# Performance work log

Hardware: AMD Instinct MI355X
Metric: run time of the kernel (lower is better)

## Reference

```python
import jax, jax.numpy as jnp
import numpy as np
from jax import lax

DIM = 512          # input channels
H_IN = 56          # input spatial size
B = 32             # batch
C = DIM // 4       # inner attention dim = 128
WS = H_IN // 4     # window size = 14
NH = 4             # num_heads (C > 64 branch)
HD = C // NH       # head dim = 32
N = WS * WS        # tokens = 196
BN_EPS = 1e-5


def _rel_index():
    # Swin-style relative position index, matches the torch buffer computation.
    coords = np.stack(np.meshgrid(np.arange(WS), np.arange(WS), indexing='ij'))  # [2,WS,WS]
    flat = coords.reshape(2, -1)                                                 # [2,N]
    rel = (flat[:, :, None] - flat[:, None, :]).transpose(1, 2, 0).astype(np.int64)  # [N,N,2]
    rel[..., 0] += WS - 1
    rel[..., 1] += WS - 1
    rel[..., 0] *= 2 * WS - 1
    return jnp.asarray(rel.sum(-1))  # [N,N] int


def _interp_mat(n_in, scale):
    # Bilinear upsample (align_corners=True, as in nn.UpsamplingBilinear2d) as a matrix.
    n_out = n_in * scale
    src = np.arange(n_out) * (n_in - 1) / (n_out - 1)
    lo = np.floor(src).astype(np.int64)
    hi = np.minimum(lo + 1, n_in - 1)
    w = (src - lo).astype(np.float32)
    M = np.zeros((n_out, n_in), np.float32)
    M[np.arange(n_out), lo] += 1.0 - w
    M[np.arange(n_out), hi] += w
    return jnp.asarray(M)  # [n_out, n_in]


def setup_inputs() -> dict:
    key = jax.random.key(0)
    ks = jax.random.split(key, 8)
    x = jax.random.normal(ks[0], (B, DIM, H_IN, H_IN), jnp.float32)
    # grouped 4x4/stride-4 conv: groups = C, in_per_group = DIM // C = 4 -> OIHW [C,4,4,4]
    conv_w = jax.random.normal(ks[1], (C, 4, 4, 4), jnp.float32) * 0.05
    conv_b = jnp.zeros((C,), jnp.float32)
    bn_gamma = jnp.ones((C,), jnp.float32)
    bn_beta = jnp.zeros((C,), jnp.float32)
    bn_mean = jnp.zeros((C,), jnp.float32)
    bn_var = jnp.ones((C,), jnp.float32)
    qkv_w = jax.random.normal(ks[2], (3 * C, C), jnp.float32) * (C ** -0.5)
    proj_w = jax.random.normal(ks[3], (C, C), jnp.float32) * (C ** -0.5)
    proj_b = jnp.zeros((C,), jnp.float32)
    rpb_table = jax.random.normal(ks[4], ((2 * WS - 1) ** 2, NH), jnp.float32) * 0.02
    convout_w = jax.random.normal(ks[5], (DIM, C), jnp.float32) * (C ** -0.5)
    convout_b = jnp.zeros((DIM,), jnp.float32)
    return dict(x=x, conv_w=conv_w, conv_b=conv_b, bn_gamma=bn_gamma, bn_beta=bn_beta,
                bn_mean=bn_mean, bn_var=bn_var, qkv_w=qkv_w, proj_w=proj_w, proj_b=proj_b,
                rpb_table=rpb_table, convout_w=convout_w, convout_b=convout_b)


def reference(x, conv_w, conv_b, bn_gamma, bn_beta, bn_mean, bn_var,
              qkv_w, proj_w, proj_b, rpb_table, convout_w, convout_b):
    # local_embed: grouped conv 4x4 s4 -> BN (eval) -> ReLU6
    y = lax.conv_general_dilated(x, conv_w, window_strides=(4, 4), padding='VALID',
                                 dimension_numbers=('NCHW', 'OIHW', 'NCHW'),
                                 feature_group_count=C)
    y = y + conv_b[None, :, None, None]
    scale_bn = bn_gamma * lax.rsqrt(bn_var + BN_EPS)
    y = y * scale_bn[None, :, None, None] + (bn_beta - bn_mean * scale_bn)[None, :, None, None]
    y = jnp.clip(y, 0.0, 6.0)  # ReLU6

    # flatten to tokens: [B, N, C]
    t = y.reshape(B, C, N).transpose(0, 2, 1)

    # qkv projection (no bias) -> q,k,v [B, NH, N, HD]
    qkv = (t @ qkv_w.T).reshape(B, N, 3, NH, HD).transpose(2, 0, 3, 1, 4)
    q, k, v = qkv[0], qkv[1], qkv[2]
    q = q * (HD ** -0.5)

    attn = jnp.einsum('bhnd,bhmd->bhnm', q, k)  # [B,NH,N,N]
    idx = _rel_index()                           # [N,N]
    bias = rpb_table[idx.reshape(-1)].reshape(N, N, NH).transpose(2, 0, 1)  # [NH,N,N]
    attn = jax.nn.softmax(attn + bias[None], axis=-1)

    o = jnp.einsum('bhnm,bhmd->bhnd', attn, v)  # [B,NH,N,HD]
    o = o.transpose(0, 2, 1, 3).reshape(B, N, C)
    o = o @ proj_w.T + proj_b

    # blc2bchw
    o = o.reshape(B, WS, WS, C).transpose(0, 3, 1, 2)  # [B,C,WS,WS]

    # 1x1 conv back to DIM channels
    o = jnp.einsum('oc,bchw->bohw', convout_w, o) + convout_b[None, :, None, None]

    # bilinear upsample x4, align_corners=True
    M = _interp_mat(WS, 4)  # [4*WS, WS]
    o = jnp.einsum('Oh,bchw->bcOw', M, o)
    o = jnp.einsum('Pw,bchw->bchP', M, o)
    return o  # [B, DIM, H_IN, H_IN]
```

## Files before the change

### kernel.cpp

```cpp
#include <hip/hip_runtime.h>

#define QSCALE 0.17677669529663687f

__global__ __launch_bounds__(256) void conv_embed_kernel(
    const float* __restrict__ x, const float* __restrict__ cw,
    const float* __restrict__ cb, const float* __restrict__ gam,
    const float* __restrict__ bet, const float* __restrict__ mea,
    const float* __restrict__ var, float* __restrict__ tbuf)
{
  __shared__ __align__(16) float xs[12544];
  __shared__ __align__(16) float wsm[64];
  const int c = blockIdx.x, b = blockIdx.y, tid = threadIdx.x;
  const float4* xb = (const float4*)(x + (b*512 + 4*c)*3136);
  for (int t = tid; t < 3136; t += 256) ((float4*)xs)[t] = xb[t];
  if (tid < 64) wsm[tid] = cw[c*64 + tid];
  __syncthreads();
  if (tid < 196) {
    int oy = tid / 14, ox = tid - (tid/14)*14;
    float acc = cb[c];
#pragma unroll
    for (int i = 0; i < 4; ++i)
#pragma unroll
      for (int kh = 0; kh < 4; ++kh) {
        float4 xv = *(const float4*)&xs[i*3136 + (4*oy+kh)*56 + 4*ox];
        float4 wv = *(const float4*)&wsm[i*16 + kh*4];
        acc += xv.x*wv.x + xv.y*wv.y + xv.z*wv.z + xv.w*wv.w;
      }
    float sc = gam[c] * rsqrtf(var[c] + 1e-5f);
    float v = acc*sc + (bet[c] - mea[c]*sc);
    v = fminf(fmaxf(v, 0.0f), 6.0f);
    tbuf[(b*196 + tid)*128 + c] = v;
  }
}

__global__ __launch_bounds__(256) void make_wc_kernel(
    const float* __restrict__ cow, const float* __restrict__ pw,
    const float* __restrict__ pb, const float* __restrict__ cob,
    float* __restrict__ Wc, float* __restrict__ bias_c)
{
  int idx = blockIdx.x*256 + threadIdx.x;
  int oc = idx >> 7, k = idx & 127;
  float acc = 0.f;
  for (int cc = 0; cc < 128; ++cc) acc += cow[oc*128 + cc] * pw[cc*128 + k];
  Wc[idx] = acc;
  if (blockIdx.x < 2) {
    float a2 = cob[idx];
    for (int cc = 0; cc < 128; ++cc) a2 += cow[idx*128 + cc] * pb[cc];
    bias_c[idx] = a2;
  }
}

__device__ __forceinline__ void gemm_tile_64x64(
    const float* __restrict__ Ag, const float* __restrict__ Bg,
    int row0, int col0, float* As, float* Bs, float (&acc)[4][4])
{
  const int tid = threadIdx.x;
#pragma unroll
  for (int it = 0; it < 8; ++it) {
    int rr = (it & 3)*16 + (tid & 15);
    int kq = (it >> 2)*16 + (tid >> 4);
    float4 va = *(const float4*)&Ag[(row0+rr)*128 + kq*4];
    As[(4*kq+0)*68 + rr] = va.x;
    As[(4*kq+1)*68 + rr] = va.y;
    As[(4*kq+2)*68 + rr] = va.z;
    As[(4*kq+3)*68 + rr] = va.w;
    float4 vb = *(const float4*)&Bg[(col0+rr)*128 + kq*4];
    Bs[(4*kq+0)*68 + rr] = vb.x;
    Bs[(4*kq+1)*68 + rr] = vb.y;
    Bs[(4*kq+2)*68 + rr] = vb.z;
    Bs[(4*kq+3)*68 + rr] = vb.w;
  }
  __syncthreads();
  const int tx = (tid & 15)*4, ty = (tid >> 4)*4;
#pragma unroll 8
  for (int k = 0; k < 128; ++k) {
    float4 a4 = *(const float4*)&As[k*68 + ty];
    float4 b4 = *(const float4*)&Bs[k*68 + tx];
    float av[4] = {a4.x, a4.y, a4.z, a4.w};
    float bv[4] = {b4.x, b4.y, b4.z, b4.w};
#pragma unroll
    for (int i = 0; i < 4; ++i)
#pragma unroll
      for (int j = 0; j < 4; ++j) acc[i][j] += av[i]*bv[j];
  }
}

__global__ __launch_bounds__(256) void gemm_qkv_kernel(
    const float* __restrict__ t, const float* __restrict__ qkv_w,
    float* __restrict__ qkv)
{
  __shared__ __align__(16) float As[128*68];
  __shared__ __align__(16) float Bs[128*68];
  float acc[4][4] = {};
  gemm_tile_64x64(t, qkv_w, blockIdx.y*64, blockIdx.x*64, As, Bs, acc);
  const int tid = threadIdx.x;
  const int tx = (tid & 15)*4, ty = (tid >> 4)*4;
  const int col0 = blockIdx.x*64 + tx;
  const int s3 = col0 >> 7, rr = col0 & 127;
  const int hh = rr >> 5, dd = rr & 31;
  const float qs = (s3 == 0) ? QSCALE : 1.0f;
#pragma unroll
  for (int i = 0; i < 4; ++i) {
    int row = blockIdx.y*64 + ty + i;
    int bb = row / 196, nn = row - bb*196;
    float4 v;
    v.x = acc[i][0]*qs; v.y = acc[i][1]*qs; v.z = acc[i][2]*qs; v.w = acc[i][3]*qs;
    *(float4*)&qkv[(((s3*32 + bb)*4 + hh)*196 + nn)*32 + dd] = v;
  }
}

__global__ __launch_bounds__(256) void attn_kernel(
    const float* __restrict__ qkv, const float* __restrict__ rpb,
    float* __restrict__ o)
{
  __shared__ __align__(16) float k_lds[196*32];
  __shared__ __align__(16) float v_lds[196*32];
  __shared__ float rpb_lds[729];
  __shared__ int   off_lds[196];
  const int qhalf = blockIdx.x, h = blockIdx.y, b = blockIdx.z;
  const int tid = threadIdx.x;
  const float4* kg = (const float4*)(qkv + ((32 + b)*4 + h)*6272);
  const float4* vg = (const float4*)(qkv + ((64 + b)*4 + h)*6272);
  for (int t = tid; t < 1568; t += 256) {
    ((float4*)k_lds)[t] = kg[t];
    ((float4*)v_lds)[t] = vg[t];
  }
  for (int t = tid; t < 729; t += 256) rpb_lds[t] = rpb[t*4 + h];
  if (tid < 196) { int y = tid/14; off_lds[tid] = y*27 + (tid - y*14); }

  const int r = tid >> 1, half = tid & 1;
  const bool act = (r < 98);
  const int n = qhalf*98 + (act ? r : 0);
  const float4* qg = (const float4*)(qkv + ((b*4 + h)*196 + n)*32);
  float4 qv[8];
#pragma unroll
  for (int d = 0; d < 8; ++d) qv[d] = qg[d];
  const int yn = n/14, xn = n - yn*14;
  const int basen = yn*27 + xn + 364;
  __syncthreads();

  float mx = -1e30f, sum = 0.f;
  float4 oa[8];
#pragma unroll
  for (int d = 0; d < 8; ++d) oa[d] = make_float4(0.f, 0.f, 0.f, 0.f);
  const int m0 = half*98;
#pragma unroll 2
  for (int i = 0; i < 98; ++i) {
    const int m = m0 + i;
    const float4* kr = (const float4*)&k_lds[m*32];
    float sx = 0.f, sy = 0.f, sz = 0.f, sw = 0.f;
#pragma unroll
    for (int d = 0; d < 8; ++d) {
      float4 kv = kr[d];
      sx += qv[d].x*kv.x; sy += qv[d].y*kv.y;
      sz += qv[d].z*kv.z; sw += qv[d].w*kv.w;
    }
    float s = (sx + sy) + (sz + sw) + rpb_lds[basen - off_lds[m]];
    if (s > mx + 4.f) {
      float sc = __expf(mx - s);
      sum *= sc;
#pragma unroll
      for (int d = 0; d < 8; ++d) {
        oa[d].x *= sc; oa[d].y *= sc; oa[d].z *= sc; oa[d].w *= sc;
      }
      mx = s;
    }
    float e = __expf(s - mx);
    sum += e;
    const float4* vr = (const float4*)&v_lds[m*32];
#pragma unroll
    for (int d = 0; d < 8; ++d) {
      float4 vv = vr[d];
      oa[d].x += e*vv.x; oa[d].y += e*vv.y;
      oa[d].z += e*vv.z; oa[d].w += e*vv.w;
    }
  }
  float omx  = __shfl_xor(mx, 1);
  float osum = __shfl_xor(sum, 1);
  float M = fmaxf(mx, omx);
  float sa = __expf(mx - M), sb = __expf(omx - M);
  float inv = 1.f / (sum*sa + osum*sb);
  sa *= inv; sb *= inv;
#pragma unroll
  for (int d = 0; d < 8; ++d) {
    float px = __shfl_xor(oa[d].x, 1);
    float py = __shfl_xor(oa[d].y, 1);
    float pz = __shfl_xor(oa[d].z, 1);
    float pw = __shfl_xor(oa[d].w, 1);
    oa[d].x = oa[d].x*sa + px*sb;
    oa[d].y = oa[d].y*sa + py*sb;
    oa[d].z = oa[d].z*sa + pz*sb;
    oa[d].w = oa[d].w*sa + pw*sb;
  }
  if (act && half == 0) {
    float4* op = (float4*)&o[(b*196 + n)*128 + h*32];
#pragma unroll
    for (int d = 0; d < 8; ++d) op[d] = oa[d];
  }
}

__global__ __launch_bounds__(256) void gemm_out_kernel(
    const float* __restrict__ obuf, const float* __restrict__ Wc,
    const float* __restrict__ bias_c, float* __restrict__ co)
{
  __shared__ __align__(16) float As[128*68];
  __shared__ __align__(16) float Bs[128*68];
  float acc[4][4] = {};
  gemm_tile_64x64(obuf, Wc, blockIdx.y*64, blockIdx.x*64, As, Bs, acc);
  const int tid = threadIdx.x;
  const int tx = (tid & 15)*4, ty = (tid >> 4)*4;
  const int row0 = blockIdx.y*64 + ty;
  const int bb = row0 / 196, nn0 = row0 - bb*196;
#pragma unroll
  for (int j = 0; j < 4; ++j) {
    int col = blockIdx.x*64 + tx + j;
    float bc = bias_c[col];
    float4 v;
    v.x = acc[0][j] + bc; v.y = acc[1][j] + bc;
    v.z = acc[2][j] + bc; v.w = acc[3][j] + bc;
    *(float4*)&co[(bb*512 + col)*196 + nn0] = v;
  }
}

__global__ __launch_bounds__(256) void upsample_kernel(
    const float* __restrict__ co, float* __restrict__ out)
{
  __shared__ float cs[1568];
  __shared__ int lo_s[56];
  __shared__ float w_s[56];
  const int cg = blockIdx.x, b = blockIdx.y, tid = threadIdx.x;
  const float* cbase = co + (b*512 + cg*8)*196;
  for (int t = tid; t < 1568; t += 256) cs[t] = cbase[t];
  if (tid < 56) {
    double s = (double)(tid*13) / 55.0;
    int lo = (int)s;
    lo_s[tid] = lo;
    w_s[tid] = (float)(s - lo);
  }
  __syncthreads();
  float* obase = out + (b*512 + cg*8)*3136;
  for (int t4 = tid; t4 < 6272; t4 += 256) {
    int ch = t4 / 784;
    int rem = t4 - ch*784;
    int i2 = rem / 14;
    int j4 = (rem - i2*14)*4;
    int li = lo_s[i2]; float wi = w_s[i2];
    int hi = (li+1 < 13) ? li+1 : 13;
    const float* p0 = cs + ch*196 + li*14;
    const float* p1 = cs + ch*196 + hi*14;
    float4 ov;
    float* ovp = (float*)&ov;
#pragma unroll
    for (int jj = 0; jj < 4; ++jj) {
      int j2 = j4 + jj;
      int lj = lo_s[j2]; float wj = w_s[j2];
      int hj = (lj+1 < 13) ? lj+1 : 13;
      float top = p0[lj]*(1.f-wj) + p0[hj]*wj;
      float bot = p1[lj]*(1.f-wj) + p1[hj]*wj;
      ovp[jj] = top*(1.f-wi) + bot*wi;
    }
    ((float4*)obase)[t4] = ov;
  }
}

extern "C" void kernel_launch(void* const* d_in, const int* in_sizes, int n_in,
                              void* d_out, int out_size, void* d_ws, size_t ws_size,
                              hipStream_t stream)
{
  const float* x         = (const float*)d_in[0];
  const float* conv_w    = (const float*)d_in[1];
  const float* conv_b    = (const float*)d_in[2];
  const float* bn_gamma  = (const float*)d_in[3];
  const float* bn_beta   = (const float*)d_in[4];
  const float* bn_mean   = (const float*)d_in[5];
  const float* bn_var    = (const float*)d_in[6];
  const float* qkv_w     = (const float*)d_in[7];
  const float* proj_w    = (const float*)d_in[8];
  const float* proj_b    = (const float*)d_in[9];
  const float* rpb       = (const float*)d_in[10];
  const float* convout_w = (const float*)d_in[11];
  const float* convout_b = (const float*)d_in[12];
  float* out = (float*)d_out;
  float* ws  = (float*)d_ws;

  float* tbuf   = ws;
  float* qkvb   = ws + 802816;
  float* obuf   = ws + 3211264;
  float* Wc     = ws + 4014080;
  float* bias_c = ws + 4079616;
  float* co     = ws + 4080128;

  conv_embed_kernel<<<dim3(128, 32), 256, 0, stream>>>(
      x, conv_w, conv_b, bn_gamma, bn_beta, bn_mean, bn_var, tbuf);
  make_wc_kernel<<<dim3(256), 256, 0, stream>>>(
      convout_w, proj_w, proj_b, convout_b, Wc, bias_c);
  gemm_qkv_kernel<<<dim3(6, 98), 256, 0, stream>>>(tbuf, qkv_w, qkvb);
  attn_kernel<<<dim3(2, 4, 32), 256, 0, stream>>>(qkvb, rpb, obuf);
  gemm_out_kernel<<<dim3(8, 98), 256, 0, stream>>>(obuf, Wc, bias_c, co);
  upsample_kernel<<<dim3(64, 32), 256, 0, stream>>>(co, out);
}
```

Baseline: 482.0 us.

## Use split-bf16 MFMA for the qkv and output projection GEMMs

```diff
diff --git a/kernel.cpp b/kernel.cpp
--- a/kernel.cpp
+++ b/kernel.cpp
@@ -1,6 +1,9 @@
 #include <hip/hip_runtime.h>
 
 #define QSCALE 0.17677669529663687f
+
+typedef __attribute__((ext_vector_type(8))) short bf16x8;
+typedef __attribute__((ext_vector_type(4))) float f32x4;
 
 __global__ __launch_bounds__(256) void conv_embed_kernel(
     const float* __restrict__ x, const float* __restrict__ cw,
@@ -50,38 +53,64 @@
   }
 }
 
-__device__ __forceinline__ void gemm_tile_64x64(
+__device__ __forceinline__ unsigned short f2bf(float f)
+{
+  unsigned u = __float_as_uint(f);
+  u += 0x7fffu + ((u >> 16) & 1u);
+  return (unsigned short)(u >> 16);
+}
+
+__device__ __forceinline__ void stage64x128(
+    const float* __restrict__ g, unsigned short* hi, unsigned short* lo, int tid)
+{
+#pragma unroll
+  for (int i = 0; i < 8; ++i) {
+    int idx4 = tid + i*256;
+    int row = idx4 >> 5;
+    int c4  = idx4 & 31;
+    float4 v = *(const float4*)&g[idx4*4];
+    ushort4 h, l;
+    h.x = f2bf(v.x); h.y = f2bf(v.y); h.z = f2bf(v.z); h.w = f2bf(v.w);
+    l.x = f2bf(v.x - __uint_as_float((unsigned)h.x << 16));
+    l.y = f2bf(v.y - __uint_as_float((unsigned)h.y << 16));
+    l.z = f2bf(v.z - __uint_as_float((unsigned)h.z << 16));
+    l.w = f2bf(v.w - __uint_as_float((unsigned)h.w << 16));
+    int slot = (c4 >> 1) ^ (row & 7);
+    int uidx = row*128 + slot*8 + (c4 & 1)*4;
+    *(ushort4*)&hi[uidx] = h;
+    *(ushort4*)&lo[uidx] = l;
+  }
+}
+
+__device__ __forceinline__ bf16x8 ldfrag(const unsigned short* p, int row, int kb)
+{
+  return *(const bf16x8*)&p[row*128 + (kb ^ (row & 7))*8];
+}
+
+__device__ __forceinline__ void mfma_tile_64x64(
     const float* __restrict__ Ag, const float* __restrict__ Bg,
-    int row0, int col0, float* As, float* Bs, float (&acc)[4][4])
+    unsigned short* Ahi, unsigned short* Alo,
+    unsigned short* Bhi, unsigned short* Blo, f32x4 (&acc)[4])
 {
   const int tid = threadIdx.x;
-#pragma unroll
-  for (int it = 0; it < 8; ++it) {
-    int rr = (it & 3)*16 + (tid & 15);
-    int kq = (it >> 2)*16 + (tid >> 4);
-    float4 va = *(const float4*)&Ag[(row0+rr)*128 + kq*4];
-    As[(4*kq+0)*68 + rr] = va.x;
-    As[(4*kq+1)*68 + rr] = va.y;
-    As[(4*kq+2)*68 + rr] = va.z;
-    As[(4*kq+3)*68 + rr] = va.w;
-    float4 vb = *(const float4*)&Bg[(col0+rr)*128 + kq*4];
-    Bs[(4*kq+0)*68 + rr] = vb.x;
-    Bs[(4*kq+1)*68 + rr] = vb.y;
-    Bs[(4*kq+2)*68 + rr] = vb.z;
-    Bs[(4*kq+3)*68 + rr] = vb.w;
-  }
-  __syncthreads();
-  const int tx = (tid & 15)*4, ty = (tid >> 4)*4;
-#pragma unroll 8
-  for (int k = 0; k < 128; ++k) {
-    float4 a4 = *(const float4*)&As[k*68 + ty];
-    float4 b4 = *(const float4*)&Bs[k*68 + tx];
-    float av[4] = {a4.x, a4.y, a4.z, a4.w};
-    float bv[4] = {b4.x, b4.y, b4.z, b4.w};
-#pragma unroll
-    for (int i = 0; i < 4; ++i)
-#pragma unroll
-      for (int j = 0; j < 4; ++j) acc[i][j] += av[i]*bv[j];
+  stage64x128(Ag, Ahi, Alo, tid);
+  stage64x128(Bg, Bhi, Blo, tid);
+  __syncthreads();
+  const int w = tid >> 6, l = tid & 63;
+  const int lr = l & 15, lg = l >> 4;
+#pragma unroll
+  for (int s = 0; s < 4; ++s) {
+    int kb = s*4 + lg;
+    bf16x8 ah = ldfrag(Ahi, w*16 + lr, kb);
+    bf16x8 al = ldfrag(Alo, w*16 + lr, kb);
+#pragma unroll
+    for (int f = 0; f < 4; ++f) {
+      bf16x8 bh = ldfrag(Bhi, f*16 + lr, kb);
+      bf16x8 bl = ldfrag(Blo, f*16 + lr, kb);
+      acc[f] = __builtin_amdgcn_mfma_f32_16x16x32_bf16(ah, bh, acc[f], 0, 0, 0);
+      acc[f] = __builtin_amdgcn_mfma_f32_16x16x32_bf16(ah, bl, acc[f], 0, 0, 0);
+      acc[f] = __builtin_amdgcn_mfma_f32_16x16x32_bf16(al, bh, acc[f], 0, 0, 0);
+    }
   }
 }
 
@@ -89,23 +118,29 @@
     const float* __restrict__ t, const float* __restrict__ qkv_w,
     float* __restrict__ qkv)
 {
-  __shared__ __align__(16) float As[128*68];
-  __shared__ __align__(16) float Bs[128*68];
-  float acc[4][4] = {};
-  gemm_tile_64x64(t, qkv_w, blockIdx.y*64, blockIdx.x*64, As, Bs, acc);
+  __shared__ __align__(16) unsigned short sm[32768];
+  unsigned short* Ahi = sm;
+  unsigned short* Alo = sm + 8192;
+  unsigned short* Bhi = sm + 16384;
+  unsigned short* Blo = sm + 24576;
+  const int m0 = blockIdx.y*64, n0 = blockIdx.x*64;
+  f32x4 acc[4] = {};
+  mfma_tile_64x64(t + m0*128, qkv_w + n0*128, Ahi, Alo, Bhi, Blo, acc);
   const int tid = threadIdx.x;
-  const int tx = (tid & 15)*4, ty = (tid >> 4)*4;
-  const int col0 = blockIdx.x*64 + tx;
-  const int s3 = col0 >> 7, rr = col0 & 127;
-  const int hh = rr >> 5, dd = rr & 31;
-  const float qs = (s3 == 0) ? QSCALE : 1.0f;
-#pragma unroll
-  for (int i = 0; i < 4; ++i) {
-    int row = blockIdx.y*64 + ty + i;
-    int bb = row / 196, nn = row - bb*196;
-    float4 v;
-    v.x = acc[i][0]*qs; v.y = acc[i][1]*qs; v.z = acc[i][2]*qs; v.w = acc[i][3]*qs;
-    *(float4*)&qkv[(((s3*32 + bb)*4 + hh)*196 + nn)*32 + dd] = v;
+  const int w = tid >> 6, l = tid & 63;
+  const int lr = l & 15, lg = l >> 4;
+#pragma unroll
+  for (int f = 0; f < 4; ++f) {
+    int col = n0 + f*16 + lr;
+    int s3 = col >> 7, rr = col & 127;
+    int hh = rr >> 5, dd = rr & 31;
+    float qs = (s3 == 0) ? QSCALE : 1.0f;
+#pragma unroll
+    for (int r = 0; r < 4; ++r) {
+      int row = m0 + w*16 + lg*4 + r;
+      int bb = row / 196, nn = row - bb*196;
+      qkv[(((s3*32 + bb)*4 + hh)*196 + nn)*32 + dd] = acc[f][r]*qs;
+    }
   }
 }
 
@@ -203,22 +238,38 @@
     const float* __restrict__ obuf, const float* __restrict__ Wc,
     const float* __restrict__ bias_c, float* __restrict__ co)
 {
-  __shared__ __align__(16) float As[128*68];
-  __shared__ __align__(16) float Bs[128*68];
-  float acc[4][4] = {};
-  gemm_tile_64x64(obuf, Wc, blockIdx.y*64, blockIdx.x*64, As, Bs, acc);
+  __shared__ __align__(16) unsigned short sm[32768];
+  unsigned short* Ahi = sm;
+  unsigned short* Alo = sm + 8192;
+  unsigned short* Bhi = sm + 16384;
+  unsigned short* Blo = sm + 24576;
+  float* tr = (float*)sm;
+  const int m0 = blockIdx.y*64, n0 = blockIdx.x*64;
+  f32x4 acc[4] = {};
+  mfma_tile_64x64(obuf + m0*128, Wc + n0*128, Ahi, Alo, Bhi, Blo, acc);
   const int tid = threadIdx.x;
-  const int tx = (tid & 15)*4, ty = (tid >> 4)*4;
-  const int row0 = blockIdx.y*64 + ty;
-  const int bb = row0 / 196, nn0 = row0 - bb*196;
-#pragma unroll
-  for (int j = 0; j < 4; ++j) {
-    int col = blockIdx.x*64 + tx + j;
-    float bc = bias_c[col];
+  const int w = tid >> 6, l = tid & 63;
+  const int lr = l & 15, lg = l >> 4;
+  __syncthreads();
+#pragma unroll
+  for (int f = 0; f < 4; ++f)
+#pragma unroll
+    for (int r = 0; r < 4; ++r)
+      tr[(w*16 + lg*4 + r)*68 + f*16 + lr] = acc[f][r];
+  __syncthreads();
+#pragma unroll
+  for (int p = 0; p < 4; ++p) {
+    int colL = p*16 + (tid >> 4);
+    int nq = tid & 15;
+    int rowG = m0 + nq*4;
+    int bb = rowG / 196, nn = rowG - bb*196;
+    float bc = bias_c[n0 + colL];
     float4 v;
-    v.x = acc[0][j] + bc; v.y = acc[1][j] + bc;
-    v.z = acc[2][j] + bc; v.w = acc[3][j] + bc;
-    *(float4*)&co[(bb*512 + col)*196 + nn0] = v;
+    v.x = tr[(nq*4+0)*68 + colL] + bc;
+    v.y = tr[(nq*4+1)*68 + colL] + bc;
+    v.z = tr[(nq*4+2)*68 + colL] + bc;
+    v.w = tr[(nq*4+3)*68 + colL] + bc;
+    *(float4*)&co[(bb*512 + n0 + colL)*196 + nn] = v;
   }
 }
 
```

New measurement: 464.4 us. 3.6% less time.
